# Optimization experiments

Hardware: AMD Instinct MI355X
Metric: run time of the kernel (lower is better)

The kernel has to match this reference:

```python
import jax, jax.numpy as jnp
import numpy as np

N = 8192
IN, HID, NH, TOT = 64, 64, 4, 128
DH = TOT // NH  # 32


def setup_inputs() -> dict:
    key = jax.random.key(0)
    ks = jax.random.split(key, 8)
    s = 0.05
    return {
        "input": jax.random.normal(ks[0], (N, IN), jnp.float32),
        "hx": jax.random.normal(ks[1], (N, HID), jnp.float32),
        "Wq": jax.random.normal(ks[2], (NH, TOT, DH), jnp.float32) * s,
        "Wk": jax.random.normal(ks[3], (NH, TOT, DH), jnp.float32) * s,
        "Wr": jax.random.normal(ks[4], (TOT, HID), jnp.float32) * s,
        "br": jnp.zeros((HID,), jnp.float32),
        "Wz": jax.random.normal(ks[5], (TOT, HID), jnp.float32) * s,
        "bz": jnp.zeros((HID,), jnp.float32),
        "Wh": jax.random.normal(ks[6], (TOT, HID), jnp.float32) * s,
        "bh": jnp.zeros((HID,), jnp.float32),
    }


def _dyn_adj(x, Wq, Wk):
    # x: [N, T]; multi-head attention adjacency, averaged over heads -> [N, N]
    q = jnp.einsum('nt,htd->hnd', x, Wq)
    k = jnp.einsum('nt,htd->hnd', x, Wk)
    scores = jnp.einsum('hnd,hmd->hnm', q, k) / jnp.sqrt(jnp.float32(DH))
    return jnp.mean(jax.nn.softmax(scores, axis=-1), axis=0)  # [N, N]


def reference(input, hx, Wq, Wk, Wr, br, Wz, bz, Wh, bh):
    x = jnp.concatenate([input, hx], axis=1)          # [N, TOT]
    adj = _dyn_adj(x, Wq, Wk)                         # [N, N] row-stochastic
    ax = adj @ x                                      # shared adjacency application
    r = jax.nn.sigmoid(ax @ Wr + br)                  # [N, HID]
    z = jax.nn.sigmoid(ax @ Wz + bz)                  # [N, HID]
    x2 = jnp.concatenate([input, r * hx], axis=1)     # [N, TOT]
    h = jnp.tanh((adj @ x2) @ Wh + bh)                # [N, HID]
    return z * hx + (1.0 - z) * h
```

## Files before the change

### kernel.cpp

```cpp
#include <hip/hip_runtime.h>
#include <hip/hip_bf16.h>

#define NN 8192
#define TOTD 128
#define HIDD 64
#define NHEAD 4
#define DHD 32
#define NCQ 16
#define JPB (NN / 32 / NCQ)

typedef __attribute__((ext_vector_type(8))) short short8;
typedef __attribute__((ext_vector_type(4))) float f32x4;

__device__ __forceinline__ short f2b(float f) {
  unsigned u = __builtin_bit_cast(unsigned, f);
  u += 0x7fff + ((u >> 16) & 1);
  return (short)(u >> 16);
}
__device__ __forceinline__ short f2b_fast(float f) {
  unsigned u = __builtin_bit_cast(unsigned, f);
  return (short)((u + 0x8000u) >> 16);
}
__device__ __forceinline__ float fexp2(float x) {
#if __has_builtin(__builtin_amdgcn_exp2f)
  return __builtin_amdgcn_exp2f(x);
#else
  return exp2f(x);
#endif
}


__global__ void k_build_xfrag(const float* __restrict__ in, const float* __restrict__ hx,
                              short* __restrict__ xb) {
  int i = blockIdx.x * 256 + threadIdx.x;
  int n = i >> 7;
  int t = i & 127;
  float v = (t < 64) ? in[n * 64 + t] : hx[n * 64 + (t - 64)];
  int jt = n >> 5, m = n & 31, cg = t >> 4;
  int l = (((m >> 2) & 3) << 4) | (t & 15);
  int e = ((m >> 4) << 2) | (m & 3);
  xb[(((size_t)jt * 8 + cg) << 9) + (l << 3) + e] = f2b(v);
}

__global__ void k_qk(const float* __restrict__ in, const float* __restrict__ hx,
                     const float* __restrict__ Wq, const float* __restrict__ Wk,
                     short* __restrict__ qb, short* __restrict__ kb) {
  __shared__ float xr[TOTD];
  int n = blockIdx.x;
  int tid = threadIdx.x;
  if (tid < TOTD) xr[tid] = (tid < 64) ? in[n * 64 + tid] : hx[n * 64 + (tid - 64)];
  __syncthreads();
  int which = tid >> 7;
  int h = (tid >> 5) & 3;
  int d = tid & 31;
  const float* W = (which ? Wk : Wq) + h * TOTD * DHD + d;
  float acc = 0.f;
#pragma unroll
  for (int t = 0; t < TOTD; ++t) acc += xr[t] * W[t * DHD];
  int l = ((d >> 3) << 4) | (n & 15);
  if (!which) {
    acc *= 0.25503486f;
    qb[(((size_t)(n >> 4) * 4 + h) << 9) + (l << 3) + (d & 7)] = f2b(acc);
  } else {
    kb[((((size_t)(n >> 5) * 4 + h) * 2 + ((n >> 4) & 1)) << 9) + (l << 3) + (d & 7)] = f2b(acc);
  }
}

__global__ __launch_bounds__(256, 8) void k_denom(
    const short* __restrict__ qb, const short* __restrict__ kb,
    float* __restrict__ lpart_g) {
  const int tid = threadIdx.x;
  const int w = tid >> 6, l = tid & 63;
  const int r0 = blockIdx.x * 64 + w * 16;
  const int rtile = blockIdx.x * 4 + w;
  const int jt0 = blockIdx.y * JPB;
  const f32x4 zero4 = {0.f, 0.f, 0.f, 0.f};

  short8 qf[NHEAD];
#pragma unroll
  for (int h = 0; h < NHEAD; ++h)
    qf[h] = *(const short8*)&qb[(((size_t)rtile * 4 + h) << 9) + l * 8];

  float acc[NHEAD] = {0.f, 0.f, 0.f, 0.f};

  for (int j = 0; j < JPB; ++j) {
    const short* kbase = kb + (((size_t)(jt0 + j) * 8) << 9) + l * 8;
#pragma unroll
    for (int h = 0; h < NHEAD; ++h) {
      short8 kf0 = *(const short8*)&kbase[(h * 2 + 0) << 9];
      short8 kf1 = *(const short8*)&kbase[(h * 2 + 1) << 9];
      f32x4 s0 = __builtin_amdgcn_mfma_f32_16x16x32_bf16(kf0, qf[h], zero4, 0, 0, 0);
      f32x4 s1 = __builtin_amdgcn_mfma_f32_16x16x32_bf16(kf1, qf[h], zero4, 0, 0, 0);
#pragma unroll
      for (int r = 0; r < 4; ++r) acc[h] += fexp2(s0[r]) + fexp2(s1[r]);
    }
  }
#pragma unroll
  for (int h = 0; h < NHEAD; ++h) {
    acc[h] += __shfl_xor(acc[h], 16, 64);
    acc[h] += __shfl_xor(acc[h], 32, 64);
  }
  if (l < 16) {
#pragma unroll
    for (int h = 0; h < NHEAD; ++h)
      lpart_g[((size_t)blockIdx.y * NHEAD + h) * NN + r0 + l] = acc[h];
  }
}

__global__ void k_linv(const float* __restrict__ lpart_g, float* __restrict__ linv_g) {
  int i = blockIdx.x * 256 + threadIdx.x;
  float s = 0.f;
#pragma unroll
  for (int q = 0; q < NCQ; ++q) s += lpart_g[(size_t)q * NHEAD * NN + i];
  linv_g[i] = 0.25f / s;
}

__global__ __launch_bounds__(256, 4) void k_pv1(
    const short* __restrict__ qb, const short* __restrict__ kb,
    const short* __restrict__ xb, const float* __restrict__ linv_g,
    float* __restrict__ axq) {
  const int tid = threadIdx.x;
  const int w = tid >> 6, l = tid & 63;
  const int col = l & 15, grp = l >> 4;
  const int r0 = blockIdx.x * 64 + w * 16;
  const int rtile = blockIdx.x * 4 + w;
  const int jt0 = blockIdx.y * JPB;
  const f32x4 zero4 = {0.f, 0.f, 0.f, 0.f};

  short8 qf[NHEAD];
#pragma unroll
  for (int h = 0; h < NHEAD; ++h)
    qf[h] = *(const short8*)&qb[(((size_t)rtile * 4 + h) << 9) + l * 8];
  float linv[NHEAD];
#pragma unroll
  for (int h = 0; h < NHEAD; ++h) linv[h] = linv_g[h * NN + r0 + col];

  f32x4 axa[8];
#pragma unroll
  for (int cg = 0; cg < 8; ++cg) axa[cg] = zero4;

  for (int j = 0; j < JPB; ++j) {
    const size_t jt = jt0 + j;
    const short* kbase = kb + ((jt * 8) << 9) + l * 8;
    const short* xbase = xb + ((jt * 8) << 9) + l * 8;
    short8 xv0 = *(const short8*)&xbase[0 << 9];
    short8 xv1 = *(const short8*)&xbase[1 << 9];
    short8 xv2 = *(const short8*)&xbase[2 << 9];
    short8 xv3 = *(const short8*)&xbase[3 << 9];
    short8 xv4 = *(const short8*)&xbase[4 << 9];
    short8 xv5 = *(const short8*)&xbase[5 << 9];
    short8 xv6 = *(const short8*)&xbase[6 << 9];
    short8 xv7 = *(const short8*)&xbase[7 << 9];
    float p[8] = {0.f, 0.f, 0.f, 0.f, 0.f, 0.f, 0.f, 0.f};
#pragma unroll
    for (int h = 0; h < NHEAD; ++h) {
      short8 kf0 = *(const short8*)&kbase[(h * 2 + 0) << 9];
      short8 kf1 = *(const short8*)&kbase[(h * 2 + 1) << 9];
      f32x4 s0 = __builtin_amdgcn_mfma_f32_16x16x32_bf16(kf0, qf[h], zero4, 0, 0, 0);
      f32x4 s1 = __builtin_amdgcn_mfma_f32_16x16x32_bf16(kf1, qf[h], zero4, 0, 0, 0);
#pragma unroll
      for (int r = 0; r < 4; ++r) {
        p[r]     += fexp2(s0[r]) * linv[h];
        p[4 + r] += fexp2(s1[r]) * linv[h];
      }
    }
    short8 pa;
#pragma unroll
    for (int e = 0; e < 8; ++e) pa[e] = f2b_fast(p[e]);
    axa[0] = __builtin_amdgcn_mfma_f32_16x16x32_bf16(pa, xv0, axa[0], 0, 0, 0);
    axa[1] = __builtin_amdgcn_mfma_f32_16x16x32_bf16(pa, xv1, axa[1], 0, 0, 0);
    axa[2] = __builtin_amdgcn_mfma_f32_16x16x32_bf16(pa, xv2, axa[2], 0, 0, 0);
    axa[3] = __builtin_amdgcn_mfma_f32_16x16x32_bf16(pa, xv3, axa[3], 0, 0, 0);
    axa[4] = __builtin_amdgcn_mfma_f32_16x16x32_bf16(pa, xv4, axa[4], 0, 0, 0);
    axa[5] = __builtin_amdgcn_mfma_f32_16x16x32_bf16(pa, xv5, axa[5], 0, 0, 0);
    axa[6] = __builtin_amdgcn_mfma_f32_16x16x32_bf16(pa, xv6, axa[6], 0, 0, 0);
    axa[7] = __builtin_amdgcn_mfma_f32_16x16x32_bf16(pa, xv7, axa[7], 0, 0, 0);
  }
#pragma unroll
  for (int cg = 0; cg < 8; ++cg)
#pragma unroll
    for (int r = 0; r < 4; ++r)
      axq[(size_t)blockIdx.y * NN * TOTD + (size_t)(r0 + grp * 4 + r) * TOTD + cg * 16 + col] =
          axa[cg][r];
}

__global__ void k_rz(const float* __restrict__ axq, const float* __restrict__ hx,
                     const float* __restrict__ Wr, const float* __restrict__ br,
                     const float* __restrict__ Wz, const float* __restrict__ bz,
                     float* __restrict__ ax, float* __restrict__ z,
                     short* __restrict__ v2f) {
  __shared__ float axs[2][TOTD];
  int tid = threadIdx.x;
  int rr = tid >> 7;
  int c2 = tid & 127;
  int n = blockIdx.x * 2 + rr;
  float s = 0.f;
#pragma unroll
  for (int q = 0; q < NCQ; ++q) s += axq[(size_t)q * NN * TOTD + (size_t)n * TOTD + c2];
  axs[rr][c2] = s;
  ax[(size_t)n * TOTD + c2] = s;
  __syncthreads();
  bool isz = c2 >= HIDD;
  int c = c2 & (HIDD - 1);
  const float* W = isz ? Wz : Wr;
  float acc = isz ? bz[c] : br[c];
#pragma unroll
  for (int t = 0; t < TOTD; ++t) acc += axs[rr][t] * W[t * HIDD + c];
  float sg = 1.f / (1.f + __expf(-acc));
  if (isz) {
    z[n * HIDD + c] = sg;
  } else {
    int jt = n >> 5, m = n & 31, cg = c >> 4;
    int ll = (((m >> 2) & 3) << 4) | (c & 15);
    int e = ((m >> 4) << 2) | (m & 3);
    v2f[(((size_t)jt * 4 + cg) << 9) + (ll << 3) + e] = f2b(sg * hx[n * HIDD + c]);
  }
}

__global__ __launch_bounds__(256, 4) void k_pv2(
    const short* __restrict__ qb, const short* __restrict__ kb,
    const short* __restrict__ v2f, const float* __restrict__ linv_g,
    float* __restrict__ a2q) {
  const int tid = threadIdx.x;
  const int w = tid >> 6, l = tid & 63;
  const int col = l & 15, grp = l >> 4;
  const int r0 = blockIdx.x * 64 + w * 16;
  const int rtile = blockIdx.x * 4 + w;
  const int jt0 = blockIdx.y * JPB;
  const f32x4 zero4 = {0.f, 0.f, 0.f, 0.f};

  short8 qf[NHEAD];
#pragma unroll
  for (int h = 0; h < NHEAD; ++h)
    qf[h] = *(const short8*)&qb[(((size_t)rtile * 4 + h) << 9) + l * 8];
  float linv[NHEAD];
#pragma unroll
  for (int h = 0; h < NHEAD; ++h) linv[h] = linv_g[h * NN + r0 + col];

  f32x4 a2a[4];
#pragma unroll
  for (int cg = 0; cg < 4; ++cg) a2a[cg] = zero4;

  for (int j = 0; j < JPB; ++j) {
    const size_t jt = jt0 + j;
    const short* kbase = kb + ((jt * 8) << 9) + l * 8;
    const short* vbase = v2f + ((jt * 4) << 9) + l * 8;
    short8 vv0 = *(const short8*)&vbase[0 << 9];
    short8 vv1 = *(const short8*)&vbase[1 << 9];
    short8 vv2 = *(const short8*)&vbase[2 << 9];
    short8 vv3 = *(const short8*)&vbase[3 << 9];
    float p[8] = {0.f, 0.f, 0.f, 0.f, 0.f, 0.f, 0.f, 0.f};
#pragma unroll
    for (int h = 0; h < NHEAD; ++h) {
      short8 kf0 = *(const short8*)&kbase[(h * 2 + 0) << 9];
      short8 kf1 = *(const short8*)&kbase[(h * 2 + 1) << 9];
      f32x4 s0 = __builtin_amdgcn_mfma_f32_16x16x32_bf16(kf0, qf[h], zero4, 0, 0, 0);
      f32x4 s1 = __builtin_amdgcn_mfma_f32_16x16x32_bf16(kf1, qf[h], zero4, 0, 0, 0);
#pragma unroll
      for (int r = 0; r < 4; ++r) {
        p[r]     += fexp2(s0[r]) * linv[h];
        p[4 + r] += fexp2(s1[r]) * linv[h];
      }
    }
    short8 pa;
#pragma unroll
    for (int e = 0; e < 8; ++e) pa[e] = f2b_fast(p[e]);
    a2a[0] = __builtin_amdgcn_mfma_f32_16x16x32_bf16(pa, vv0, a2a[0], 0, 0, 0);
    a2a[1] = __builtin_amdgcn_mfma_f32_16x16x32_bf16(pa, vv1, a2a[1], 0, 0, 0);
    a2a[2] = __builtin_amdgcn_mfma_f32_16x16x32_bf16(pa, vv2, a2a[2], 0, 0, 0);
    a2a[3] = __builtin_amdgcn_mfma_f32_16x16x32_bf16(pa, vv3, a2a[3], 0, 0, 0);
  }
#pragma unroll
  for (int cg = 0; cg < 4; ++cg)
#pragma unroll
    for (int r = 0; r < 4; ++r)
      a2q[(size_t)blockIdx.y * NN * HIDD + (size_t)(r0 + grp * 4 + r) * HIDD + cg * 16 + col] =
          a2a[cg][r];
}

__global__ __launch_bounds__(256) void k_final(
    const float* __restrict__ a2q, const float* __restrict__ ax,
    const float* __restrict__ hx, const float* __restrict__ Wh,
    const float* __restrict__ bh, const float* __restrict__ z,
    float* __restrict__ out) {
  __shared__ float Whs[TOTD * HIDD];
  __shared__ float a2s[16][HIDD];
  const int tid = threadIdx.x;
  const int r0 = blockIdx.x * 16;

  for (int i = tid; i < TOTD * HIDD; i += 256) Whs[i] = Wh[i];
  for (int i = tid; i < 16 * HIDD; i += 256) {
    int rw = i >> 6, c = i & 63;
    size_t gi = (size_t)(r0 + rw) * HIDD + c;
    float s = 0.f;
#pragma unroll
    for (int q = 0; q < NCQ; ++q) s += a2q[(size_t)q * NN * HIDD + gi];
    a2s[rw][c] = s;
  }
  __syncthreads();
  for (int o = tid; o < 16 * HIDD; o += 256) {
    int rw = o >> 6, c = o & 63;
    const float* axrow = &ax[(size_t)(r0 + rw) * TOTD];
    float acc = bh[c];
#pragma unroll
    for (int t = 0; t < 64; ++t) acc += axrow[t] * Whs[t * HIDD + c];
#pragma unroll
    for (int t = 0; t < 64; ++t) acc += a2s[rw][t] * Whs[(64 + t) * HIDD + c];
    float hval = tanhf(acc);
    size_t gi = (size_t)(r0 + rw) * HIDD + c;
    float zz = z[gi];
    out[gi] = zz * hx[gi] + (1.f - zz) * hval;
  }
}

extern "C" void kernel_launch(void* const* d_in, const int* in_sizes, int n_in,
                              void* d_out, int out_size, void* d_ws, size_t ws_size,
                              hipStream_t stream) {
  const float* in = (const float*)d_in[0];
  const float* hx = (const float*)d_in[1];
  const float* Wq = (const float*)d_in[2];
  const float* Wk = (const float*)d_in[3];
  const float* Wr = (const float*)d_in[4];
  const float* br = (const float*)d_in[5];
  const float* Wz = (const float*)d_in[6];
  const float* bz = (const float*)d_in[7];
  const float* Wh = (const float*)d_in[8];
  const float* bh = (const float*)d_in[9];

  const size_t MB = 1ull << 20;
  char* ws = (char*)d_ws;
  short* qb    = (short*)(ws + 0 * MB);
  short* kb    = (short*)(ws + 2 * MB);
  short* xb    = (short*)(ws + 4 * MB);
  float* linv  = (float*)(ws + 6 * MB);
  float* lpart = (float*)(ws + 7 * MB);
  float* ax    = (float*)(ws + 10 * MB);
  float* z     = (float*)(ws + 14 * MB);
  short* v2f   = (short*)(ws + 16 * MB);
  float* axq   = (float*)(ws + 20 * MB);
  float* a2q   = (float*)(ws + 84 * MB);
  float* out   = (float*)d_out;

  k_build_xfrag<<<dim3((NN * TOTD) / 256), dim3(256), 0, stream>>>(in, hx, xb);
  k_qk<<<dim3(NN), dim3(256), 0, stream>>>(in, hx, Wq, Wk, qb, kb);
  k_denom<<<dim3(NN / 64, NCQ), dim3(256), 0, stream>>>(qb, kb, lpart);
  k_linv<<<dim3((NHEAD * NN) / 256), dim3(256), 0, stream>>>(lpart, linv);
  k_pv1<<<dim3(NN / 64, NCQ), dim3(256), 0, stream>>>(qb, kb, xb, linv, axq);
  k_rz<<<dim3(NN / 2), dim3(256), 0, stream>>>(axq, hx, Wr, br, Wz, bz, ax, z, v2f);
  k_pv2<<<dim3(NN / 64, NCQ), dim3(256), 0, stream>>>(qb, kb, v2f, linv, a2q);
  k_final<<<dim3(NN / 16), dim3(256), 0, stream>>>(a2q, ax, hx, Wh, bh, z, out);
}
```

Before: 247.8 us.

## Switch attention kernels to 32x32x16 MFMA tiles and batch QK projection

```diff
diff --git a/kernel.cpp b/kernel.cpp
--- a/kernel.cpp
+++ b/kernel.cpp
@@ -11,6 +11,7 @@
 
 typedef __attribute__((ext_vector_type(8))) short short8;
 typedef __attribute__((ext_vector_type(4))) float f32x4;
+typedef __attribute__((ext_vector_type(16))) float f32x16;
 
 __device__ __forceinline__ short f2b(float f) {
   unsigned u = __builtin_bit_cast(unsigned, f);
@@ -28,6 +29,12 @@
   return exp2f(x);
 #endif
 }
+__device__ __forceinline__ f32x16 zero16() {
+  f32x16 z;
+#pragma unroll
+  for (int i = 0; i < 16; ++i) z[i] = 0.f;
+  return z;
+}
 
 
 __global__ void k_build_xfrag(const float* __restrict__ in, const float* __restrict__ hx,
@@ -36,50 +43,81 @@
   int n = i >> 7;
   int t = i & 127;
   float v = (t < 64) ? in[n * 64 + t] : hx[n * 64 + (t - 64)];
-  int jt = n >> 5, m = n & 31, cg = t >> 4;
-  int l = (((m >> 2) & 3) << 4) | (t & 15);
-  int e = ((m >> 4) << 2) | (m & 3);
-  xb[(((size_t)jt * 8 + cg) << 9) + (l << 3) + e] = f2b(v);
-}
-
-__global__ void k_qk(const float* __restrict__ in, const float* __restrict__ hx,
-                     const float* __restrict__ Wq, const float* __restrict__ Wk,
-                     short* __restrict__ qb, short* __restrict__ kb) {
-  __shared__ float xr[TOTD];
-  int n = blockIdx.x;
-  int tid = threadIdx.x;
-  if (tid < TOTD) xr[tid] = (tid < 64) ? in[n * 64 + tid] : hx[n * 64 + (tid - 64)];
-  __syncthreads();
-  int which = tid >> 7;
-  int h = (tid >> 5) & 3;
-  int d = tid & 31;
-  const float* W = (which ? Wk : Wq) + h * TOTD * DHD + d;
-  float acc = 0.f;
-#pragma unroll
-  for (int t = 0; t < TOTD; ++t) acc += xr[t] * W[t * DHD];
-  int l = ((d >> 3) << 4) | (n & 15);
-  if (!which) {
-    acc *= 0.25503486f;
-    qb[(((size_t)(n >> 4) * 4 + h) << 9) + (l << 3) + (d & 7)] = f2b(acc);
-  } else {
-    kb[((((size_t)(n >> 5) * 4 + h) * 2 + ((n >> 4) & 1)) << 9) + (l << 3) + (d & 7)] = f2b(acc);
-  }
-}
-
-__global__ __launch_bounds__(256, 8) void k_denom(
+  int jt = n >> 5, nn = n & 31;
+  int m = nn >> 4, rem = nn & 15;
+  int hi = (rem >> 2) & 1;
+  int e = (rem & 3) | ((rem >> 3) << 2);
+  int ct = t >> 5;
+  int lane = (hi << 5) | (t & 31);
+  xb[(((size_t)jt * 8 + ct * 2 + m) << 9) + (lane << 3) + e] = f2b(v);
+}
+
+__global__ __launch_bounds__(256, 2) void k_qk(
+    const float* __restrict__ in, const float* __restrict__ hx,
+    const float* __restrict__ Wq, const float* __restrict__ Wk,
+    short* __restrict__ qb, short* __restrict__ kb) {
+  __shared__ float Ws[32 * 256];
+  __shared__ float xr_t[128 * 16];
+  const int tid = threadIdx.x;
+  const int n0 = blockIdx.x * 16;
+  for (int i = tid; i < 2048; i += 256) {
+    int r = i & 15, t = i >> 4;
+    xr_t[t * 16 + r] = (t < 64) ? in[(n0 + r) * 64 + t] : hx[(n0 + r) * 64 + (t - 64)];
+  }
+  const int which = tid >> 7;
+  const int h = (tid >> 5) & 3;
+  const int d = tid & 31;
+  const int c = tid;
+  float acc[16];
+#pragma unroll
+  for (int r = 0; r < 16; ++r) acc[r] = 0.f;
+
+  for (int pass = 0; pass < 4; ++pass) {
+    __syncthreads();
+    for (int i = tid; i < 32 * 256; i += 256) {
+      int tt = pass * 32 + (i >> 8);
+      int cc = i & 255;
+      const float* W = (cc < 128) ? Wq : Wk;
+      int hh = (cc >> 5) & 3, dd = cc & 31;
+      Ws[(i >> 8) * 256 + cc] = W[((size_t)hh * 128 + tt) * 32 + dd];
+    }
+    __syncthreads();
+#pragma unroll
+    for (int t = 0; t < 32; ++t) {
+      float wv = Ws[t * 256 + c];
+      const float4* xp = (const float4*)&xr_t[(pass * 32 + t) * 16];
+      float4 x0 = xp[0], x1 = xp[1], x2 = xp[2], x3 = xp[3];
+      acc[0] += x0.x * wv;  acc[1] += x0.y * wv;  acc[2] += x0.z * wv;  acc[3] += x0.w * wv;
+      acc[4] += x1.x * wv;  acc[5] += x1.y * wv;  acc[6] += x1.z * wv;  acc[7] += x1.w * wv;
+      acc[8] += x2.x * wv;  acc[9] += x2.y * wv;  acc[10] += x2.z * wv; acc[11] += x2.w * wv;
+      acc[12] += x3.x * wv; acc[13] += x3.y * wv; acc[14] += x3.z * wv; acc[15] += x3.w * wv;
+    }
+  }
+#pragma unroll
+  for (int r = 0; r < 16; ++r) {
+    int n = n0 + r;
+    int lane = (((d >> 3) & 1) << 5) | (n & 31);
+    size_t idx = ((((size_t)(n >> 5) * 4 + h) * 2 + (d >> 4)) << 9) + (lane << 3) + (d & 7);
+    if (which == 0) qb[idx] = f2b(acc[r] * 0.25503486f);
+    else            kb[idx] = f2b(acc[r]);
+  }
+}
+
+__global__ __launch_bounds__(256, 4) void k_denom(
     const short* __restrict__ qb, const short* __restrict__ kb,
     float* __restrict__ lpart_g) {
   const int tid = threadIdx.x;
   const int w = tid >> 6, l = tid & 63;
-  const int r0 = blockIdx.x * 64 + w * 16;
-  const int rtile = blockIdx.x * 4 + w;
+  const int r0 = blockIdx.x * 128 + w * 32;
+  const int rt = blockIdx.x * 4 + w;
   const int jt0 = blockIdx.y * JPB;
-  const f32x4 zero4 = {0.f, 0.f, 0.f, 0.f};
-
-  short8 qf[NHEAD];
+
+  short8 qf[NHEAD][2];
 #pragma unroll
   for (int h = 0; h < NHEAD; ++h)
-    qf[h] = *(const short8*)&qb[(((size_t)rtile * 4 + h) << 9) + l * 8];
+#pragma unroll
+    for (int m = 0; m < 2; ++m)
+      qf[h][m] = *(const short8*)&qb[((((size_t)rt * 4 + h) * 2 + m) << 9) + l * 8];
 
   float acc[NHEAD] = {0.f, 0.f, 0.f, 0.f};
 
@@ -89,18 +127,15 @@
     for (int h = 0; h < NHEAD; ++h) {
       short8 kf0 = *(const short8*)&kbase[(h * 2 + 0) << 9];
       short8 kf1 = *(const short8*)&kbase[(h * 2 + 1) << 9];
-      f32x4 s0 = __builtin_amdgcn_mfma_f32_16x16x32_bf16(kf0, qf[h], zero4, 0, 0, 0);
-      f32x4 s1 = __builtin_amdgcn_mfma_f32_16x16x32_bf16(kf1, qf[h], zero4, 0, 0, 0);
-#pragma unroll
-      for (int r = 0; r < 4; ++r) acc[h] += fexp2(s0[r]) + fexp2(s1[r]);
-    }
-  }
-#pragma unroll
-  for (int h = 0; h < NHEAD; ++h) {
-    acc[h] += __shfl_xor(acc[h], 16, 64);
-    acc[h] += __shfl_xor(acc[h], 32, 64);
-  }
-  if (l < 16) {
+      f32x16 s = __builtin_amdgcn_mfma_f32_32x32x16_bf16(kf0, qf[h][0], zero16(), 0, 0, 0);
+      s = __builtin_amdgcn_mfma_f32_32x32x16_bf16(kf1, qf[h][1], s, 0, 0, 0);
+#pragma unroll
+      for (int r = 0; r < 16; ++r) acc[h] += fexp2(s[r]);
+    }
+  }
+#pragma unroll
+  for (int h = 0; h < NHEAD; ++h) acc[h] += __shfl_xor(acc[h], 32, 64);
+  if (l < 32) {
 #pragma unroll
     for (int h = 0; h < NHEAD; ++h)
       lpart_g[((size_t)blockIdx.y * NHEAD + h) * NN + r0 + l] = acc[h];
@@ -115,73 +150,68 @@
   linv_g[i] = 0.25f / s;
 }
 
-__global__ __launch_bounds__(256, 4) void k_pv1(
+__global__ __launch_bounds__(256, 2) void k_pv1(
     const short* __restrict__ qb, const short* __restrict__ kb,
     const short* __restrict__ xb, const float* __restrict__ linv_g,
     float* __restrict__ axq) {
   const int tid = threadIdx.x;
   const int w = tid >> 6, l = tid & 63;
-  const int col = l & 15, grp = l >> 4;
-  const int r0 = blockIdx.x * 64 + w * 16;
-  const int rtile = blockIdx.x * 4 + w;
+  const int hi = l >> 5, col = l & 31;
+  const int r0 = blockIdx.x * 128 + w * 32;
+  const int rt = blockIdx.x * 4 + w;
   const int jt0 = blockIdx.y * JPB;
-  const f32x4 zero4 = {0.f, 0.f, 0.f, 0.f};
-
-  short8 qf[NHEAD];
+
+  short8 qf[NHEAD][2];
 #pragma unroll
   for (int h = 0; h < NHEAD; ++h)
-    qf[h] = *(const short8*)&qb[(((size_t)rtile * 4 + h) << 9) + l * 8];
+#pragma unroll
+    for (int m = 0; m < 2; ++m)
+      qf[h][m] = *(const short8*)&qb[((((size_t)rt * 4 + h) * 2 + m) << 9) + l * 8];
   float linv[NHEAD];
 #pragma unroll
   for (int h = 0; h < NHEAD; ++h) linv[h] = linv_g[h * NN + r0 + col];
 
-  f32x4 axa[8];
-#pragma unroll
-  for (int cg = 0; cg < 8; ++cg) axa[cg] = zero4;
+  f32x16 axa[4];
+#pragma unroll
+  for (int ct = 0; ct < 4; ++ct) axa[ct] = zero16();
 
   for (int j = 0; j < JPB; ++j) {
     const size_t jt = jt0 + j;
     const short* kbase = kb + ((jt * 8) << 9) + l * 8;
     const short* xbase = xb + ((jt * 8) << 9) + l * 8;
-    short8 xv0 = *(const short8*)&xbase[0 << 9];
-    short8 xv1 = *(const short8*)&xbase[1 << 9];
-    short8 xv2 = *(const short8*)&xbase[2 << 9];
-    short8 xv3 = *(const short8*)&xbase[3 << 9];
-    short8 xv4 = *(const short8*)&xbase[4 << 9];
-    short8 xv5 = *(const short8*)&xbase[5 << 9];
-    short8 xv6 = *(const short8*)&xbase[6 << 9];
-    short8 xv7 = *(const short8*)&xbase[7 << 9];
-    float p[8] = {0.f, 0.f, 0.f, 0.f, 0.f, 0.f, 0.f, 0.f};
+    short8 xv[8];
+#pragma unroll
+    for (int cchunk = 0; cchunk < 8; ++cchunk)
+      xv[cchunk] = *(const short8*)&xbase[cchunk << 9];
+    float p[16];
+#pragma unroll
+    for (int r = 0; r < 16; ++r) p[r] = 0.f;
 #pragma unroll
     for (int h = 0; h < NHEAD; ++h) {
       short8 kf0 = *(const short8*)&kbase[(h * 2 + 0) << 9];
       short8 kf1 = *(const short8*)&kbase[(h * 2 + 1) << 9];
-      f32x4 s0 = __builtin_amdgcn_mfma_f32_16x16x32_bf16(kf0, qf[h], zero4, 0, 0, 0);
-      f32x4 s1 = __builtin_amdgcn_mfma_f32_16x16x32_bf16(kf1, qf[h], zero4, 0, 0, 0);
-#pragma unroll
-      for (int r = 0; r < 4; ++r) {
-        p[r]     += fexp2(s0[r]) * linv[h];
-        p[4 + r] += fexp2(s1[r]) * linv[h];
-      }
-    }
-    short8 pa;
-#pragma unroll
-    for (int e = 0; e < 8; ++e) pa[e] = f2b_fast(p[e]);
-    axa[0] = __builtin_amdgcn_mfma_f32_16x16x32_bf16(pa, xv0, axa[0], 0, 0, 0);
-    axa[1] = __builtin_amdgcn_mfma_f32_16x16x32_bf16(pa, xv1, axa[1], 0, 0, 0);
-    axa[2] = __builtin_amdgcn_mfma_f32_16x16x32_bf16(pa, xv2, axa[2], 0, 0, 0);
-    axa[3] = __builtin_amdgcn_mfma_f32_16x16x32_bf16(pa, xv3, axa[3], 0, 0, 0);
-    axa[4] = __builtin_amdgcn_mfma_f32_16x16x32_bf16(pa, xv4, axa[4], 0, 0, 0);
-    axa[5] = __builtin_amdgcn_mfma_f32_16x16x32_bf16(pa, xv5, axa[5], 0, 0, 0);
-    axa[6] = __builtin_amdgcn_mfma_f32_16x16x32_bf16(pa, xv6, axa[6], 0, 0, 0);
-    axa[7] = __builtin_amdgcn_mfma_f32_16x16x32_bf16(pa, xv7, axa[7], 0, 0, 0);
-  }
-#pragma unroll
-  for (int cg = 0; cg < 8; ++cg)
-#pragma unroll
-    for (int r = 0; r < 4; ++r)
-      axq[(size_t)blockIdx.y * NN * TOTD + (size_t)(r0 + grp * 4 + r) * TOTD + cg * 16 + col] =
-          axa[cg][r];
+      f32x16 s = __builtin_amdgcn_mfma_f32_32x32x16_bf16(kf0, qf[h][0], zero16(), 0, 0, 0);
+      s = __builtin_amdgcn_mfma_f32_32x32x16_bf16(kf1, qf[h][1], s, 0, 0, 0);
+#pragma unroll
+      for (int r = 0; r < 16; ++r) p[r] += fexp2(s[r]) * linv[h];
+    }
+    short8 pa0, pa1;
+#pragma unroll
+    for (int e = 0; e < 8; ++e) { pa0[e] = f2b_fast(p[e]); pa1[e] = f2b_fast(p[8 + e]); }
+#pragma unroll
+    for (int ct = 0; ct < 4; ++ct) {
+      axa[ct] = __builtin_amdgcn_mfma_f32_32x32x16_bf16(pa0, xv[ct * 2 + 0], axa[ct], 0, 0, 0);
+      axa[ct] = __builtin_amdgcn_mfma_f32_32x32x16_bf16(pa1, xv[ct * 2 + 1], axa[ct], 0, 0, 0);
+    }
+  }
+#pragma unroll
+  for (int ct = 0; ct < 4; ++ct)
+#pragma unroll
+    for (int r = 0; r < 16; ++r) {
+      int row = (r & 3) + 8 * (r >> 2) + 4 * hi;
+      axq[(size_t)blockIdx.y * NN * TOTD + (size_t)(r0 + row) * TOTD + ct * 32 + col] =
+          axa[ct][r];
+    }
 }
 
 __global__ void k_rz(const float* __restrict__ axq, const float* __restrict__ hx,
@@ -210,72 +240,78 @@
   if (isz) {
     z[n * HIDD + c] = sg;
   } else {
-    int jt = n >> 5, m = n & 31, cg = c >> 4;
-    int ll = (((m >> 2) & 3) << 4) | (c & 15);
-    int e = ((m >> 4) << 2) | (m & 3);
-    v2f[(((size_t)jt * 4 + cg) << 9) + (ll << 3) + e] = f2b(sg * hx[n * HIDD + c]);
-  }
-}
-
-__global__ __launch_bounds__(256, 4) void k_pv2(
+    int jt = n >> 5, nn = n & 31;
+    int m = nn >> 4, rem = nn & 15;
+    int hi = (rem >> 2) & 1;
+    int e = (rem & 3) | ((rem >> 3) << 2);
+    int ct = c >> 5;
+    int lane = (hi << 5) | (c & 31);
+    v2f[(((size_t)jt * 4 + ct * 2 + m) << 9) + (lane << 3) + e] = f2b(sg * hx[n * HIDD + c]);
+  }
+}
+
+__global__ __launch_bounds__(256, 3) void k_pv2(
     const short* __restrict__ qb, const short* __restrict__ kb,
     const short* __restrict__ v2f, const float* __restrict__ linv_g,
     float* __restrict__ a2q) {
   const int tid = threadIdx.x;
   const int w = tid >> 6, l = tid & 63;
-  const int col = l & 15, grp = l >> 4;
-  const int r0 = blockIdx.x * 64 + w * 16;
-  const int rtile = blockIdx.x * 4 + w;
+  const int hi = l >> 5, col = l & 31;
+  const int r0 = blockIdx.x * 128 + w * 32;
+  const int rt = blockIdx.x * 4 + w;
   const int jt0 = blockIdx.y * JPB;
-  const f32x4 zero4 = {0.f, 0.f, 0.f, 0.f};
-
-  short8 qf[NHEAD];
+
+  short8 qf[NHEAD][2];
 #pragma unroll
   for (int h = 0; h < NHEAD; ++h)
-    qf[h] = *(const short8*)&qb[(((size_t)rtile * 4 + h) << 9) + l * 8];
+#pragma unroll
+    for (int m = 0; m < 2; ++m)
+      qf[h][m] = *(const short8*)&qb[((((size_t)rt * 4 + h) * 2 + m) << 9) + l * 8];
   float linv[NHEAD];
 #pragma unroll
   for (int h = 0; h < NHEAD; ++h) linv[h] = linv_g[h * NN + r0 + col];
 
-  f32x4 a2a[4];
-#pragma unroll
-  for (int cg = 0; cg < 4; ++cg) a2a[cg] = zero4;
+  f32x16 a2a[2];
+#pragma unroll
+  for (int ct = 0; ct < 2; ++ct) a2a[ct] = zero16();
 
   for (int j = 0; j < JPB; ++j) {
     const size_t jt = jt0 + j;
     const short* kbase = kb + ((jt * 8) << 9) + l * 8;
     const short* vbase = v2f + ((jt * 4) << 9) + l * 8;
-    short8 vv0 = *(const short8*)&vbase[0 << 9];
-    short8 vv1 = *(const short8*)&vbase[1 << 9];
-    short8 vv2 = *(const short8*)&vbase[2 << 9];
-    short8 vv3 = *(const short8*)&vbase[3 << 9];
-    float p[8] = {0.f, 0.f, 0.f, 0.f, 0.f, 0.f, 0.f, 0.f};
+    short8 vv[4];
+#pragma unroll
+    for (int cchunk = 0; cchunk < 4; ++cchunk)
+      vv[cchunk] = *(const short8*)&vbase[cchunk << 9];
+    float p[16];
+#pragma unroll
+    for (int r = 0; r < 16; ++r) p[r] = 0.f;
 #pragma unroll
     for (int h = 0; h < NHEAD; ++h) {
       short8 kf0 = *(const short8*)&kbase[(h * 2 + 0) << 9];
       short8 kf1 = *(const short8*)&kbase[(h * 2 + 1) << 9];
-      f32x4 s0 = __builtin_amdgcn_mfma_f32_16x16x32_bf16(kf0, qf[h], zero4, 0, 0, 0);
-      f32x4 s1 = __builtin_amdgcn_mfma_f32_16x16x32_bf16(kf1, qf[h], zero4, 0, 0, 0);
-#pragma unroll
-      for (int r = 0; r < 4; ++r) {
-        p[r]     += fexp2(s0[r]) * linv[h];
-        p[4 + r] += fexp2(s1[r]) * linv[h];
-      }
-    }
-    short8 pa;
-#pragma unroll
-    for (int e = 0; e < 8; ++e) pa[e] = f2b_fast(p[e]);
-    a2a[0] = __builtin_amdgcn_mfma_f32_16x16x32_bf16(pa, vv0, a2a[0], 0, 0, 0);
-    a2a[1] = __builtin_amdgcn_mfma_f32_16x16x32_bf16(pa, vv1, a2a[1], 0, 0, 0);
-    a2a[2] = __builtin_amdgcn_mfma_f32_16x16x32_bf16(pa, vv2, a2a[2], 0, 0, 0);
-    a2a[3] = __builtin_amdgcn_mfma_f32_16x16x32_bf16(pa, vv3, a2a[3], 0, 0, 0);
-  }
-#pragma unroll
-  for (int cg = 0; cg < 4; ++cg)
-#pragma unroll
-    for (int r = 0; r < 4; ++r)
-      a2q[(size_t)blockIdx.y * NN * HIDD + (size_t)(r0 + grp * 4 + r) * HIDD + cg * 16 + col] =
-          a2a[cg][r];
+      f32x16 s = __builtin_amdgcn_mfma_f32_32x32x16_bf16(kf0, qf[h][0], zero16(), 0, 0, 0);
+      s = __builtin_amdgcn_mfma_f32_32x32x16_bf16(kf1, qf[h][1], s, 0, 0, 0);
+#pragma unroll
+      for (int r = 0; r < 16; ++r) p[r] += fexp2(s[r]) * linv[h];
+    }
+    short8 pa0, pa1;
+#pragma unroll
+    for (int e = 0; e < 8; ++e) { pa0[e] = f2b_fast(p[e]); pa1[e] = f2b_fast(p[8 + e]); }
+#pragma unroll
+    for (int ct = 0; ct < 2; ++ct) {
+      a2a[ct] = __builtin_amdgcn_mfma_f32_32x32x16_bf16(pa0, vv[ct * 2 + 0], a2a[ct], 0, 0, 0);
+      a2a[ct] = __builtin_amdgcn_mfma_f32_32x32x16_bf16(pa1, vv[ct * 2 + 1], a2a[ct], 0, 0, 0);
+    }
+  }
+#pragma unroll
+  for (int ct = 0; ct < 2; ++ct)
+#pragma unroll
+    for (int r = 0; r < 16; ++r) {
+      int row = (r & 3) + 8 * (r >> 2) + 4 * hi;
+      a2q[(size_t)blockIdx.y * NN * HIDD + (size_t)(r0 + row) * HIDD + ct * 32 + col] =
+          a2a[ct][r];
+    }
 }
 
 __global__ __launch_bounds__(256) void k_final(
@@ -342,11 +378,11 @@
   float* out   = (float*)d_out;
 
   k_build_xfrag<<<dim3((NN * TOTD) / 256), dim3(256), 0, stream>>>(in, hx, xb);
-  k_qk<<<dim3(NN), dim3(256), 0, stream>>>(in, hx, Wq, Wk, qb, kb);
-  k_denom<<<dim3(NN / 64, NCQ), dim3(256), 0, stream>>>(qb, kb, lpart);
+  k_qk<<<dim3(NN / 16), dim3(256), 0, stream>>>(in, hx, Wq, Wk, qb, kb);
+  k_denom<<<dim3(NN / 128, NCQ), dim3(256), 0, stream>>>(qb, kb, lpart);
   k_linv<<<dim3((NHEAD * NN) / 256), dim3(256), 0, stream>>>(lpart, linv);
-  k_pv1<<<dim3(NN / 64, NCQ), dim3(256), 0, stream>>>(qb, kb, xb, linv, axq);
+  k_pv1<<<dim3(NN / 128, NCQ), dim3(256), 0, stream>>>(qb, kb, xb, linv, axq);
   k_rz<<<dim3(NN / 2), dim3(256), 0, stream>>>(axq, hx, Wr, br, Wz, bz, ax, z, v2f);
-  k_pv2<<<dim3(NN / 64, NCQ), dim3(256), 0, stream>>>(qb, kb, v2f, linv, a2q);
+  k_pv2<<<dim3(NN / 128, NCQ), dim3(256), 0, stream>>>(qb, kb, v2f, linv, a2q);
   k_final<<<dim3(NN / 16), dim3(256), 0, stream>>>(a2q, ax, hx, Wh, bh, z, out);
 }
```

New measurement: 210.0 us. 1.18x faster.
